# Optimization experiments

Measured on AMD Instinct MI355X. Metric: run time of the kernel, lower is better.

Reference implementation:

```python
import jax, jax.numpy as jnp
import numpy as np

TAU = 1.0
NUM_NEURONS = 32768
INPUT_SIZE = 8192
BATCH = 512


def setup_inputs() -> dict:
    key = jax.random.key(0)
    k1, k2, k3 = jax.random.split(key, 3)
    x = jax.random.uniform(k1, (BATCH, INPUT_SIZE), dtype=jnp.float32)
    gate_weights = jax.random.normal(k2, (NUM_NEURONS, 16), dtype=jnp.float32)
    input_idx = jax.random.randint(k3, (NUM_NEURONS, 2), 0, INPUT_SIZE, dtype=jnp.int32)
    return {"x": x, "gate_weights": gate_weights, "input_idx": input_idx}


def _all_logic_ops(a, b):
    # 16 soft (real-valued) binary logic gates, stacked on last axis.
    ab = a * b
    one = jnp.ones_like(a)
    zero = jnp.zeros_like(a)
    return jnp.stack([
        zero,                  # FALSE
        ab,                    # a AND b
        a - ab,                # a AND NOT b
        a,                     # a
        b - ab,                # NOT a AND b
        b,                     # b
        a + b - 2.0 * ab,      # a XOR b
        a + b - ab,            # a OR b
        1.0 - (a + b - ab),    # NOR
        1.0 - (a + b - 2.0 * ab),  # XNOR
        1.0 - b,               # NOT b
        1.0 - b + ab,          # a OR NOT b
        1.0 - a,               # NOT a
        1.0 - a + ab,          # NOT a OR b
        1.0 - ab,              # NAND
        one,                   # TRUE
    ], axis=-1)  # (B, N, 16)


def reference(x, gate_weights, input_idx):
    # gather the two input columns per neuron: (B, N)
    a = x[:, input_idx[:, 0]]
    b = x[:, input_idx[:, 1]]
    ops = _all_logic_ops(a, b)                          # (B, N, 16)
    w = jax.nn.softmax(gate_weights / TAU, axis=1)      # (N, 16)
    out = jnp.einsum('bnk,nk->bn', ops, w)              # (B, N)
    return out
```

## Files before the change

kernel.cpp:

```cpp
#include <hip/hip_runtime.h>
#include <hip/hip_bf16.h>

#define NUM_NEURONS 32768
#define INPUT_SIZE  8192
#define BATCH       512

__global__ __launch_bounds__(256) void logic_coeff_kernel(
    const float* __restrict__ gw, float4* __restrict__ coeffs)
{
    const int n = blockIdx.x * 256 + threadIdx.x;
    if (n >= NUM_NEURONS) return;
    const float* g = gw + (size_t)n * 16;

    float w[16];
#pragma unroll
    for (int i = 0; i < 16; i += 4) {
        float4 v = *reinterpret_cast<const float4*>(g + i);
        w[i+0] = v.x; w[i+1] = v.y; w[i+2] = v.z; w[i+3] = v.w;
    }
    float m = w[0];
#pragma unroll
    for (int i = 1; i < 16; ++i) m = fmaxf(m, w[i]);
    float s = 0.f;
#pragma unroll
    for (int i = 0; i < 16; ++i) { w[i] = expf(w[i] - m); s += w[i]; }
    const float inv = 1.0f / s;

    const float C0  = (w[8] + w[9] + w[10] + w[11] + w[12] + w[13] + w[14] + w[15]) * inv;
    const float Ca  = (w[2] + w[3] + w[6] + w[7] - w[8] - w[9] - w[12] - w[13]) * inv;
    const float Cb  = (w[4] + w[5] + w[6] + w[7] - w[8] - w[9] - w[10] - w[11]) * inv;
    const float Cab = (w[1] - w[2] - w[4] - 2.f*w[6] - w[7]
                       + w[8] + 2.f*w[9] + w[11] + w[13] - w[14]) * inv;

    coeffs[n] = make_float4(C0, Ca, Cb, Cab);
}

constexpr int CHUNK = 2048;
constexpr int NPT   = CHUNK / 256;
constexpr int ROWS_PER_BLOCK = 4;

__global__ __launch_bounds__(256) void logic_main_kernel(
    const float*  __restrict__ x,
    const float4* __restrict__ coeffs,
    const int2*   __restrict__ idx,
    float*        __restrict__ out)
{
    __shared__ float sx[INPUT_SIZE];

    const int tid    = threadIdx.x;
    const int chunk0 = blockIdx.x * CHUNK;
    const int row0   = blockIdx.y * ROWS_PER_BLOCK;

    float4 c[NPT];
    int2   id[NPT];
#pragma unroll
    for (int i = 0; i < NPT; ++i) {
        const int n = chunk0 + i * 256 + tid;
        c[i]  = coeffs[n];
        id[i] = idx[n];
    }

    for (int r = 0; r < ROWS_PER_BLOCK; ++r) {
        const int row = row0 + r;
        if (r) __syncthreads();

        const float4* xrow = reinterpret_cast<const float4*>(x + (size_t)row * INPUT_SIZE);
        float4* s4 = reinterpret_cast<float4*>(sx);
#pragma unroll
        for (int i = 0; i < INPUT_SIZE / 4 / 256; ++i)
            s4[i * 256 + tid] = xrow[i * 256 + tid];
        __syncthreads();

        float* o = out + (size_t)row * NUM_NEURONS + chunk0 + tid;
#pragma unroll
        for (int i = 0; i < NPT; ++i) {
            const float a = sx[id[i].x];
            const float b = sx[id[i].y];
            o[i * 256] = c[i].x + a * (c[i].y + c[i].w * b) + c[i].z * b;
        }
    }
}

extern "C" void kernel_launch(void* const* d_in, const int* in_sizes, int n_in,
                              void* d_out, int out_size, void* d_ws, size_t ws_size,
                              hipStream_t stream)
{
    const float* x   = (const float*)d_in[0];
    const float* gw  = (const float*)d_in[1];
    const int2*  idx = (const int2*)d_in[2];
    float* out = (float*)d_out;

    float4* coeffs = (float4*)d_ws;

    logic_coeff_kernel<<<NUM_NEURONS / 256, 256, 0, stream>>>(gw, coeffs);

    dim3 grid(NUM_NEURONS / CHUNK, BATCH / ROWS_PER_BLOCK);
    logic_main_kernel<<<grid, 256, 0, stream>>>(x, coeffs, idx, out);
}
```

Measured before the change: 108.8 us.

## Vectorize output stores, prefetch next x row, and remap blocks across XCDs

Each thread now handles four consecutive neurons, so coefficient and index loads become contiguous and outputs are written as float4. The next batch row of x is prefetched into registers while the current row is being computed. Blocks are launched on a 1D grid whose index is remapped so that each XCD works on a contiguous range of row groups. The chunk size doubles to 4096, which raises per-thread register use (16 float4 coefficients plus 8 float4 of prefetch) and may lower occupancy.

```diff
diff --git a/kernel.cpp b/kernel.cpp
--- a/kernel.cpp
+++ b/kernel.cpp
@@ -35,48 +35,83 @@
     coeffs[n] = make_float4(C0, Ca, Cb, Cab);
 }
 
-constexpr int CHUNK = 2048;
-constexpr int NPT   = CHUNK / 256;
+constexpr int CHUNK  = 4096;
+constexpr int NPT    = CHUNK / 256;
+constexpr int NGRP   = NPT / 4;
 constexpr int ROWS_PER_BLOCK = 4;
+constexpr int XF4    = INPUT_SIZE / 4 / 256;
+constexpr int NCHUNKS = NUM_NEURONS / CHUNK;
+constexpr int NROWG   = BATCH / ROWS_PER_BLOCK;
+constexpr int NXCD    = 8;
 
 __global__ __launch_bounds__(256) void logic_main_kernel(
     const float*  __restrict__ x,
     const float4* __restrict__ coeffs,
-    const int2*   __restrict__ idx,
-    float*        __restrict__ out)
+    const int4*   __restrict__ idx4,
+    float4*       __restrict__ out4)
 {
     __shared__ float sx[INPUT_SIZE];
 
-    const int tid    = threadIdx.x;
-    const int chunk0 = blockIdx.x * CHUNK;
-    const int row0   = blockIdx.y * ROWS_PER_BLOCK;
+    const int tid = threadIdx.x;
+
+    const int bid    = blockIdx.x;
+    const int xcd    = bid % NXCD;
+    const int within = bid / NXCD;
+    const int chunkI = within % NCHUNKS;
+    const int rowgI  = xcd * (NROWG / NXCD) + within / NCHUNKS;
+    const int chunk0 = chunkI * CHUNK;
+    const int row0   = rowgI * ROWS_PER_BLOCK;
 
     float4 c[NPT];
     int2   id[NPT];
 #pragma unroll
-    for (int i = 0; i < NPT; ++i) {
-        const int n = chunk0 + i * 256 + tid;
-        c[i]  = coeffs[n];
-        id[i] = idx[n];
+    for (int g = 0; g < NGRP; ++g) {
+        const int nbase = chunk0 + g * 1024 + tid * 4;
+#pragma unroll
+        for (int j = 0; j < 4; ++j) c[g*4+j] = coeffs[nbase + j];
+        const int4 p0 = idx4[(nbase >> 1) + 0];
+        const int4 p1 = idx4[(nbase >> 1) + 1];
+        id[g*4+0] = make_int2(p0.x, p0.y);
+        id[g*4+1] = make_int2(p0.z, p0.w);
+        id[g*4+2] = make_int2(p1.x, p1.y);
+        id[g*4+3] = make_int2(p1.z, p1.w);
     }
+
+    float4 pf[XF4];
+    {
+        const float4* xr = reinterpret_cast<const float4*>(x + (size_t)row0 * INPUT_SIZE);
+#pragma unroll
+        for (int i = 0; i < XF4; ++i) pf[i] = xr[i * 256 + tid];
+    }
+
+    float4* s4 = reinterpret_cast<float4*>(sx);
 
     for (int r = 0; r < ROWS_PER_BLOCK; ++r) {
         const int row = row0 + r;
         if (r) __syncthreads();
 
-        const float4* xrow = reinterpret_cast<const float4*>(x + (size_t)row * INPUT_SIZE);
-        float4* s4 = reinterpret_cast<float4*>(sx);
 #pragma unroll
-        for (int i = 0; i < INPUT_SIZE / 4 / 256; ++i)
-            s4[i * 256 + tid] = xrow[i * 256 + tid];
+        for (int i = 0; i < XF4; ++i) s4[i * 256 + tid] = pf[i];
         __syncthreads();
 
-        float* o = out + (size_t)row * NUM_NEURONS + chunk0 + tid;
+        if (r + 1 < ROWS_PER_BLOCK) {
+            const float4* xr = reinterpret_cast<const float4*>(x + (size_t)(row + 1) * INPUT_SIZE);
 #pragma unroll
-        for (int i = 0; i < NPT; ++i) {
-            const float a = sx[id[i].x];
-            const float b = sx[id[i].y];
-            o[i * 256] = c[i].x + a * (c[i].y + c[i].w * b) + c[i].z * b;
+            for (int i = 0; i < XF4; ++i) pf[i] = xr[i * 256 + tid];
+        }
+
+        float4* o = out4 + ((size_t)row * NUM_NEURONS + chunk0) / 4;
+#pragma unroll
+        for (int g = 0; g < NGRP; ++g) {
+            float res[4];
+#pragma unroll
+            for (int j = 0; j < 4; ++j) {
+                const float4 cc = c[g*4+j];
+                const float a = sx[id[g*4+j].x];
+                const float b = sx[id[g*4+j].y];
+                res[j] = fmaf(a, fmaf(cc.w, b, cc.y), fmaf(cc.z, b, cc.x));
+            }
+            o[g * 256 + tid] = make_float4(res[0], res[1], res[2], res[3]);
         }
     }
 }
@@ -87,13 +122,13 @@
 {
     const float* x   = (const float*)d_in[0];
     const float* gw  = (const float*)d_in[1];
-    const int2*  idx = (const int2*)d_in[2];
-    float* out = (float*)d_out;
+    const int4*  idx = (const int4*)d_in[2];
+    float4* out = (float4*)d_out;
 
     float4* coeffs = (float4*)d_ws;
 
     logic_coeff_kernel<<<NUM_NEURONS / 256, 256, 0, stream>>>(gw, coeffs);
 
-    dim3 grid(NUM_NEURONS / CHUNK, BATCH / ROWS_PER_BLOCK);
-    logic_main_kernel<<<grid, 256, 0, stream>>>(x, coeffs, idx, out);
+    const int nblocks = NCHUNKS * NROWG;
+    logic_main_kernel<<<nblocks, 256, 0, stream>>>(x, coeffs, idx, out);
 }
```

Measured after the change: 153.9 us. 1.41x slower.

## Restructure main kernel: one block per row pair, all neurons, direct LDS loads, vector stores

Applied to the files above, without the earlier changes.

The main kernel now gives each 1024-thread block two batch rows and all neurons. Both rows of x are staged into LDS with global_load_lds, and the grid shrinks to BATCH/2 blocks. Each thread handles four consecutive neurons, reading coefficients and packed index pairs as vectors, and writes float4 results with nontemporal stores. This targets the old per-block reload of x rows and the scalar output stores. The cost is that coefficients and indices are reread from global/L2 for every row pair. The softmax also switches to __expf.

```diff
diff --git a/kernel.cpp b/kernel.cpp
--- a/kernel.cpp
+++ b/kernel.cpp
@@ -4,6 +4,8 @@
 #define NUM_NEURONS 32768
 #define INPUT_SIZE  8192
 #define BATCH       512
+
+typedef float f32x4 __attribute__((ext_vector_type(4)));
 
 __global__ __launch_bounds__(256) void logic_coeff_kernel(
     const float* __restrict__ gw, float4* __restrict__ coeffs)
@@ -23,7 +25,7 @@
     for (int i = 1; i < 16; ++i) m = fmaxf(m, w[i]);
     float s = 0.f;
 #pragma unroll
-    for (int i = 0; i < 16; ++i) { w[i] = expf(w[i] - m); s += w[i]; }
+    for (int i = 0; i < 16; ++i) { w[i] = __expf(w[i] - m); s += w[i]; }
     const float inv = 1.0f / s;
 
     const float C0  = (w[8] + w[9] + w[10] + w[11] + w[12] + w[13] + w[14] + w[15]) * inv;
@@ -35,48 +37,69 @@
     coeffs[n] = make_float4(C0, Ca, Cb, Cab);
 }
 
-constexpr int CHUNK = 2048;
-constexpr int NPT   = CHUNK / 256;
-constexpr int ROWS_PER_BLOCK = 4;
+constexpr int RPB = 2;
+constexpr int BLK = 1024;
+constexpr int QPT = NUM_NEURONS / 4 / BLK;
+constexpr int SF4 = RPB * INPUT_SIZE / 4 / BLK;
 
-__global__ __launch_bounds__(256) void logic_main_kernel(
+__global__ __launch_bounds__(BLK, 4) void logic_main_kernel(
     const float*  __restrict__ x,
     const float4* __restrict__ coeffs,
-    const int2*   __restrict__ idx,
+    const int4*   __restrict__ idx4,
     float*        __restrict__ out)
 {
-    __shared__ float sx[INPUT_SIZE];
+    __shared__ float sx[RPB][INPUT_SIZE];
 
-    const int tid    = threadIdx.x;
-    const int chunk0 = blockIdx.x * CHUNK;
-    const int row0   = blockIdx.y * ROWS_PER_BLOCK;
+    const int tid  = threadIdx.x;
+    const int row0 = blockIdx.x * RPB;
 
-    float4 c[NPT];
-    int2   id[NPT];
+    {
+        const float4* xr = reinterpret_cast<const float4*>(x + (size_t)row0 * INPUT_SIZE);
+        float4* s4 = reinterpret_cast<float4*>(&sx[0][0]);
 #pragma unroll
-    for (int i = 0; i < NPT; ++i) {
-        const int n = chunk0 + i * 256 + tid;
-        c[i]  = coeffs[n];
-        id[i] = idx[n];
+        for (int i = 0; i < SF4; ++i) {
+            __builtin_amdgcn_global_load_lds(
+                (const __attribute__((address_space(1))) void*)(xr + i * BLK + tid),
+                (__attribute__((address_space(3))) void*)(s4 + i * BLK + tid),
+                16, 0, 0);
+        }
     }
+    asm volatile("s_waitcnt vmcnt(0)" ::: "memory");
+    __builtin_amdgcn_s_barrier();
 
-    for (int r = 0; r < ROWS_PER_BLOCK; ++r) {
-        const int row = row0 + r;
-        if (r) __syncthreads();
+#pragma unroll 2
+    for (int g = 0; g < QPT; ++g) {
+        const int nb = g * (BLK * 4) + tid * 4;
 
-        const float4* xrow = reinterpret_cast<const float4*>(x + (size_t)row * INPUT_SIZE);
-        float4* s4 = reinterpret_cast<float4*>(sx);
+        const float4 c0 = coeffs[nb + 0];
+        const float4 c1 = coeffs[nb + 1];
+        const float4 c2 = coeffs[nb + 2];
+        const float4 c3 = coeffs[nb + 3];
+        const int4   p0 = idx4[(nb >> 1) + 0];
+        const int4   p1 = idx4[(nb >> 1) + 1];
+
 #pragma unroll
-        for (int i = 0; i < INPUT_SIZE / 4 / 256; ++i)
-            s4[i * 256 + tid] = xrow[i * 256 + tid];
-        __syncthreads();
-
-        float* o = out + (size_t)row * NUM_NEURONS + chunk0 + tid;
-#pragma unroll
-        for (int i = 0; i < NPT; ++i) {
-            const float a = sx[id[i].x];
-            const float b = sx[id[i].y];
-            o[i * 256] = c[i].x + a * (c[i].y + c[i].w * b) + c[i].z * b;
+        for (int rr = 0; rr < RPB; ++rr) {
+            const float* s = sx[rr];
+            f32x4 res;
+            {
+                const float a = s[p0.x], b = s[p0.y];
+                res[0] = fmaf(a, fmaf(c0.w, b, c0.y), fmaf(c0.z, b, c0.x));
+            }
+            {
+                const float a = s[p0.z], b = s[p0.w];
+                res[1] = fmaf(a, fmaf(c1.w, b, c1.y), fmaf(c1.z, b, c1.x));
+            }
+            {
+                const float a = s[p1.x], b = s[p1.y];
+                res[2] = fmaf(a, fmaf(c2.w, b, c2.y), fmaf(c2.z, b, c2.x));
+            }
+            {
+                const float a = s[p1.z], b = s[p1.w];
+                res[3] = fmaf(a, fmaf(c3.w, b, c3.y), fmaf(c3.z, b, c3.x));
+            }
+            __builtin_nontemporal_store(
+                res, reinterpret_cast<f32x4*>(out + (size_t)(row0 + rr) * NUM_NEURONS + nb));
         }
     }
 }
@@ -87,13 +110,12 @@
 {
     const float* x   = (const float*)d_in[0];
     const float* gw  = (const float*)d_in[1];
-    const int2*  idx = (const int2*)d_in[2];
+    const int4*  idx = (const int4*)d_in[2];
     float* out = (float*)d_out;
 
     float4* coeffs = (float4*)d_ws;
 
     logic_coeff_kernel<<<NUM_NEURONS / 256, 256, 0, stream>>>(gw, coeffs);
 
-    dim3 grid(NUM_NEURONS / CHUNK, BATCH / ROWS_PER_BLOCK);
-    logic_main_kernel<<<grid, 256, 0, stream>>>(x, coeffs, idx, out);
+    logic_main_kernel<<<BATCH / RPB, BLK, 0, stream>>>(x, coeffs, idx, out);
 }
```

Result: faster. 94.78 us (-12.9%).
